# Kernel tuning notes

Hardware: AMD Instinct MI355X
Metric: run time of the kernel (lower is better)

Reference implementation:

```python
import jax, jax.numpy as jnp
import numpy as np

P_BINS = 5
T_BINS = 16
B_BINS = P_BINS * T_BINS  # 80
IN_CH = 16
OUT_CH = 32
N_VERTS = 30000   # mesh vertices (cols of conn)
N_PATCH = 30000   # patches (rows of conn / B)
K_NNZ = 3         # nnz per sparse row (interpolation support)


def setup_inputs() -> dict:
    key = jax.random.key(0)
    k1, k2, k3, k4 = jax.random.split(key, 4)
    x = jax.random.normal(k1, (N_VERTS, IN_CH), dtype=jnp.float32)
    conn_idx = jax.random.randint(k2, (N_PATCH * B_BINS, K_NNZ), 0, N_VERTS, dtype=jnp.int32)
    conn_val = jax.random.uniform(k3, (N_PATCH * B_BINS, K_NNZ), dtype=jnp.float32)
    weights = jax.random.normal(k4, (B_BINS, IN_CH, OUT_CH), dtype=jnp.float32)
    return {"x": x, "conn_idx": conn_idx, "conn_val": conn_val, "weights": weights}


def _rotated_weights(weights):
    # layer_weights[j, :, :, i] = weights[(j + p*i) % B]  -> reshape (B*inp, out*t)
    j = jnp.arange(B_BINS)[:, None]
    i = jnp.arange(T_BINS)[None, :]
    idx = (j + P_BINS * i) % B_BINS                       # (B, t)
    lw = weights[idx]                                     # (B, t, inp, out)
    lw = jnp.transpose(lw, (0, 2, 3, 1))                  # (B, inp, out, t)
    return lw.reshape(B_BINS * IN_CH, OUT_CH * T_BINS)


def reference(x, conn_idx, conn_val, weights):
    # sparse.mm(conn, x): gather K vertex features per bin row and weight-sum
    gathered = jnp.einsum('rk,rkc->rc', conn_val, x[conn_idx])  # (N*B, inp)
    h = gathered.reshape(-1, B_BINS * IN_CH)                    # (N, B*inp)
    lw = _rotated_weights(weights)                              # (B*inp, out*t)
    y = h @ lw                                                  # (N, out*t)
    y = y.reshape(-1, OUT_CH, T_BINS)
    return jnp.max(y, axis=-1)                                  # (N, out)
```

## Files before the change

kernel.cpp:

```cpp
#include <hip/hip_runtime.h>
#include <hip/hip_bf16.h>
#include <stdint.h>

#define NP 30000
#define BBINS 80
#define INCH 16
#define OUTCH 32
#define KDIM 1280
#define NDIM 512
#define KSTEPS 40
#define NROWS (NP * BBINS)

typedef __bf16 bf16x8 __attribute__((ext_vector_type(8)));
typedef __bf16 bf16x4 __attribute__((ext_vector_type(4)));
typedef float f32x4 __attribute__((ext_vector_type(4)));

__device__ __forceinline__ void async_ld16(const void* g, void* l) {
    __builtin_amdgcn_global_load_lds(
        (const __attribute__((address_space(1))) unsigned int*)g,
        (__attribute__((address_space(3))) unsigned int*)l,
        16, 0, 0);
}

__global__ void prep_weights(const float* __restrict__ w, __bf16* __restrict__ pw) {
    int gid = blockIdx.x * 256 + threadIdx.x;
    int e  = gid & 7;
    int qs = (gid >> 3) & 3;
    int n  = (gid >> 5) & 511;
    int kc = gid >> 14;
    int kp = kc * 32 + ((qs ^ (n & 3)) << 3) + e;
    int b = kp >> 4, c = kp & 15;
    int o = n >> 4,  t = n & 15;
    int bid = (b + 5 * t) % BBINS;
    pw[gid] = (__bf16)w[(bid * INCH + c) * OUTCH + o];
}

__global__ __launch_bounds__(256) void gather_h(
    const float* __restrict__ x,
    const int*   __restrict__ cidx,
    const float* __restrict__ cval,
    __bf16* __restrict__ h) {
    const int gid = blockIdx.x * 256 + threadIdx.x;
    const int r = gid >> 2;
    const int q = gid & 3;
    const int r3 = r * 3;
    const int i0 = cidx[r3 + 0], i1 = cidx[r3 + 1], i2 = cidx[r3 + 2];
    const float v0 = cval[r3 + 0], v1 = cval[r3 + 1], v2 = cval[r3 + 2];
    const float4 a = *(const float4*)(x + (size_t)i0 * 16 + q * 4);
    const float4 b = *(const float4*)(x + (size_t)i1 * 16 + q * 4);
    const float4 c = *(const float4*)(x + (size_t)i2 * 16 + q * 4);
    bf16x4 hv;
    hv[0] = (__bf16)(v0 * a.x + v1 * b.x + v2 * c.x);
    hv[1] = (__bf16)(v0 * a.y + v1 * b.y + v2 * c.y);
    hv[2] = (__bf16)(v0 * a.z + v1 * b.z + v2 * c.z);
    hv[3] = (__bf16)(v0 * a.w + v1 * b.w + v2 * c.w);
    *(bf16x4*)((char*)h + (size_t)gid * 8) = hv;
}

__global__ __launch_bounds__(256, 2) void gemm_max(
    const __bf16* __restrict__ h,
    const __bf16* __restrict__ pw,
    float* __restrict__ out) {

    __shared__ __align__(16) __bf16 Alds[128 * 32];
    __shared__ __align__(16) __bf16 Blds[256 * 32];

    const int bid = blockIdx.x;
    const int m    = (bid >> 4) * 8 + (bid & 7);
    const int ncol = (bid >> 3) & 1;
    if (m >= 235) return;
    const int mbase = m * 128;

    const int tid  = threadIdx.x;
    const int lane = tid & 63;
    const int wave = tid >> 6;
    const int wave_mrow = wave >> 1;
    const int wave_ncol = wave & 1;

    int a_off[4], b_off[8];
    {
        const int ml = lane & 15, q = lane >> 4;
#pragma unroll
        for (int i = 0; i < 4; ++i)
            a_off[i] = (wave_mrow * 64 + i * 16 + ml) * 64 + q * 16;
#pragma unroll
        for (int j = 0; j < 8; ++j) {
            int nl = wave_ncol * 128 + j * 16 + ml;
            b_off[j] = nl * 64 + ((q ^ (nl & 3)) << 4);
        }
    }

    f32x4 acc[4][8];
#pragma unroll
    for (int i = 0; i < 4; ++i)
#pragma unroll
        for (int j = 0; j < 8; ++j)
            acc[i][j] = (f32x4){0.f, 0.f, 0.f, 0.f};

    const char* hB  = (const char*)h;
    const char* pwB = (const char*)pw + ncol * 16384 + tid * 16;
    int rg0 = mbase + (tid >> 2);
    int rg1 = rg0 + 64;
    if (rg0 > NP - 1) rg0 = NP - 1;
    if (rg1 > NP - 1) rg1 = NP - 1;
    const char* aSrc0 = hB + (size_t)rg0 * 2560 + (tid & 3) * 16;
    const char* aSrc1 = hB + (size_t)rg1 * 2560 + (tid & 3) * 16;
    char* aDst0 = (char*)Alds + tid * 16;
    char* aDst1 = aDst0 + 4096;
    char* bDst  = (char*)Blds + tid * 16;

    for (int kc = 0; kc < KSTEPS; ++kc) {
        const char* bs = pwB + kc * 32768;
#pragma unroll
        for (int i = 0; i < 4; ++i)
            async_ld16(bs + i * 4096, bDst + i * 4096);
        async_ld16(aSrc0 + kc * 64, aDst0);
        async_ld16(aSrc1 + kc * 64, aDst1);
        __syncthreads();

        bf16x8 af[4], bfr[8];
#pragma unroll
        for (int i = 0; i < 4; ++i)
            af[i] = *(const bf16x8*)((const char*)Alds + a_off[i]);
#pragma unroll
        for (int j = 0; j < 8; ++j)
            bfr[j] = *(const bf16x8*)((const char*)Blds + b_off[j]);
#pragma unroll
        for (int i = 0; i < 4; ++i)
#pragma unroll
            for (int j = 0; j < 8; ++j)
                acc[i][j] = __builtin_amdgcn_mfma_f32_16x16x32_bf16(
                    af[i], bfr[j], acc[i][j], 0, 0, 0);
        __syncthreads();
    }

    const int rgrp = lane >> 4;
    const int tl   = lane & 15;
#pragma unroll
    for (int i = 0; i < 4; ++i) {
#pragma unroll
        for (int j = 0; j < 8; ++j) {
            float v0 = acc[i][j][0], v1 = acc[i][j][1];
            float v2 = acc[i][j][2], v3 = acc[i][j][3];
#pragma unroll
            for (int off = 1; off < 16; off <<= 1) {
                v0 = fmaxf(v0, __shfl_xor(v0, off));
                v1 = fmaxf(v1, __shfl_xor(v1, off));
                v2 = fmaxf(v2, __shfl_xor(v2, off));
                v3 = fmaxf(v3, __shfl_xor(v3, off));
            }
            if (tl == 0) {
                const int o  = ncol * 16 + wave_ncol * 8 + j;
                const int pr = mbase + wave_mrow * 64 + i * 16 + rgrp * 4;
                if (pr + 0 < NP) out[(pr + 0) * 32 + o] = v0;
                if (pr + 1 < NP) out[(pr + 1) * 32 + o] = v1;
                if (pr + 2 < NP) out[(pr + 2) * 32 + o] = v2;
                if (pr + 3 < NP) out[(pr + 3) * 32 + o] = v3;
            }
        }
    }
}

extern "C" void kernel_launch(void* const* d_in, const int* in_sizes, int n_in,
                              void* d_out, int out_size, void* d_ws, size_t ws_size,
                              hipStream_t stream) {
    const float* x    = (const float*)d_in[0];
    const int*   cidx = (const int*)d_in[1];
    const float* cval = (const float*)d_in[2];
    const float* w    = (const float*)d_in[3];
    float* out = (float*)d_out;

    __bf16* pw = (__bf16*)d_ws;
    __bf16* h  = (__bf16*)((char*)d_ws + (2 << 20));

    hipLaunchKernelGGL(prep_weights, dim3(2560), dim3(256), 0, stream, w, pw);
    hipLaunchKernelGGL(gather_h, dim3(NROWS * 4 / 256), dim3(256), 0, stream,
                       x, cidx, cval, h);
    hipLaunchKernelGGL(gemm_max, dim3(480), dim3(256), 0, stream,
                       h, (const __bf16*)pw, out);
}
```

Before: 188.8 us.

## Double-buffer GEMM LDS stages, enlarge tiles, swizzle A layout, stage gather indices in LDS

The GEMM now uses 512-thread blocks over 256-row tiles, with double-buffered A and B LDS stages, so each k-step's async loads overlap the previous step's MFMAs and one barrier per iteration is removed. The gather kernel loads each block's index and value rows into shared memory with coalesced vector loads. It also writes h in a swizzled order so A-fragment LDS reads avoid bank conflicts, and the weight swizzle is changed to the same pattern. The cost is a single barrier guarding buffer reuse, which leaves subtle races possible, plus more LDS per block, which may lower occupancy.

Result: slower. 209.9 us (+11.1%).

```diff
diff --git a/kernel.cpp b/kernel.cpp
--- a/kernel.cpp
+++ b/kernel.cpp
@@ -28,7 +28,7 @@
     int qs = (gid >> 3) & 3;
     int n  = (gid >> 5) & 511;
     int kc = gid >> 14;
-    int kp = kc * 32 + ((qs ^ (n & 3)) << 3) + e;
+    int kp = kc * 32 + ((qs ^ ((n >> 1) & 3)) << 3) + e;
     int b = kp >> 4, c = kp & 15;
     int o = n >> 4,  t = n & 15;
     int bid = (b + 5 * t) % BBINS;
@@ -40,12 +40,22 @@
     const int*   __restrict__ cidx,
     const float* __restrict__ cval,
     __bf16* __restrict__ h) {
-    const int gid = blockIdx.x * 256 + threadIdx.x;
-    const int r = gid >> 2;
-    const int q = gid & 3;
-    const int r3 = r * 3;
-    const int i0 = cidx[r3 + 0], i1 = cidx[r3 + 1], i2 = cidx[r3 + 2];
-    const float v0 = cval[r3 + 0], v1 = cval[r3 + 1], v2 = cval[r3 + 2];
+    __shared__ int   ci[192];
+    __shared__ float cv[192];
+    const int t  = threadIdx.x;
+    const int r0 = blockIdx.x * 64;
+
+    if (t < 48)
+        ((int4*)ci)[t] = ((const int4*)(cidx + (size_t)r0 * 3))[t];
+    else if (t >= 64 && t < 112)
+        ((float4*)cv)[t - 64] = ((const float4*)(cval + (size_t)r0 * 3))[t - 64];
+    __syncthreads();
+
+    const int rl = t >> 2;
+    const int q  = t & 3;
+    const int i0 = ci[rl * 3 + 0], i1 = ci[rl * 3 + 1], i2 = ci[rl * 3 + 2];
+    const float v0 = cv[rl * 3 + 0], v1 = cv[rl * 3 + 1], v2 = cv[rl * 3 + 2];
+
     const float4 a = *(const float4*)(x + (size_t)i0 * 16 + q * 4);
     const float4 b = *(const float4*)(x + (size_t)i1 * 16 + q * 4);
     const float4 c = *(const float4*)(x + (size_t)i2 * 16 + q * 4);
@@ -54,40 +64,44 @@
     hv[1] = (__bf16)(v0 * a.y + v1 * b.y + v2 * c.y);
     hv[2] = (__bf16)(v0 * a.z + v1 * b.z + v2 * c.z);
     hv[3] = (__bf16)(v0 * a.w + v1 * b.w + v2 * c.w);
-    *(bf16x4*)((char*)h + (size_t)gid * 8) = hv;
-}
-
-__global__ __launch_bounds__(256, 2) void gemm_max(
+
+    const int r   = r0 + rl;
+    const int p   = r / 80;
+    const int bin = r - p * 80;
+    const int cl  = 2 * (bin & 1) + (q >> 1);
+    const int slot = cl ^ ((p >> 1) & 3);
+    const size_t off = (size_t)p * 2560 + (bin >> 1) * 64 + slot * 16 + (q & 1) * 8;
+    *(bf16x4*)((char*)h + off) = hv;
+}
+
+__global__ __launch_bounds__(512, 2) void gemm_max(
     const __bf16* __restrict__ h,
     const __bf16* __restrict__ pw,
     float* __restrict__ out) {
 
-    __shared__ __align__(16) __bf16 Alds[128 * 32];
-    __shared__ __align__(16) __bf16 Blds[256 * 32];
-
-    const int bid = blockIdx.x;
-    const int m    = (bid >> 4) * 8 + (bid & 7);
-    const int ncol = (bid >> 3) & 1;
-    if (m >= 235) return;
-    const int mbase = m * 128;
+    __shared__ __align__(16) char Abuf[2][16384];
+    __shared__ __align__(16) char Bbuf[2][16384];
+
+    const int m    = blockIdx.x >> 1;
+    const int ncol = blockIdx.x & 1;
+    const int mbase = m * 256;
 
     const int tid  = threadIdx.x;
     const int lane = tid & 63;
     const int wave = tid >> 6;
-    const int wave_mrow = wave >> 1;
-    const int wave_ncol = wave & 1;
+    const int wm = wave >> 1;
+    const int wc = wave & 1;
 
     int a_off[4], b_off[8];
     {
         const int ml = lane & 15, q = lane >> 4;
+        const int swz = (q ^ ((ml >> 1) & 3)) << 4;
 #pragma unroll
         for (int i = 0; i < 4; ++i)
-            a_off[i] = (wave_mrow * 64 + i * 16 + ml) * 64 + q * 16;
-#pragma unroll
-        for (int j = 0; j < 8; ++j) {
-            int nl = wave_ncol * 128 + j * 16 + ml;
-            b_off[j] = nl * 64 + ((q ^ (nl & 3)) << 4);
-        }
+            a_off[i] = (wm * 64 + i * 16 + ml) * 64 + swz;
+#pragma unroll
+        for (int j = 0; j < 8; ++j)
+            b_off[j] = (wc * 128 + j * 16 + ml) * 64 + swz;
     }
 
     f32x4 acc[4][8];
@@ -97,42 +111,47 @@
         for (int j = 0; j < 8; ++j)
             acc[i][j] = (f32x4){0.f, 0.f, 0.f, 0.f};
 
-    const char* hB  = (const char*)h;
-    const char* pwB = (const char*)pw + ncol * 16384 + tid * 16;
-    int rg0 = mbase + (tid >> 2);
-    int rg1 = rg0 + 64;
-    if (rg0 > NP - 1) rg0 = NP - 1;
-    if (rg1 > NP - 1) rg1 = NP - 1;
-    const char* aSrc0 = hB + (size_t)rg0 * 2560 + (tid & 3) * 16;
-    const char* aSrc1 = hB + (size_t)rg1 * 2560 + (tid & 3) * 16;
-    char* aDst0 = (char*)Alds + tid * 16;
-    char* aDst1 = aDst0 + 4096;
-    char* bDst  = (char*)Blds + tid * 16;
+    int rA0 = mbase + (tid >> 2);
+    int rA1 = rA0 + 128;
+    if (rA0 > NP - 1) rA0 = NP - 1;
+    if (rA1 > NP - 1) rA1 = NP - 1;
+    const char* aSrc0 = (const char*)h + (size_t)rA0 * 2560 + (tid & 3) * 16;
+    const char* aSrc1 = (const char*)h + (size_t)rA1 * 2560 + (tid & 3) * 16;
+    const char* bSrc  = (const char*)pw + ncol * 16384 + tid * 16;
+    const int ldsOff  = tid * 16;
+
+#define STAGE(KC, BUF)                                                  \
+    do {                                                                \
+        async_ld16(aSrc0 + (KC) * 64, Abuf[BUF] + ldsOff);              \
+        async_ld16(aSrc1 + (KC) * 64, Abuf[BUF] + 8192 + ldsOff);       \
+        async_ld16(bSrc + (KC) * 32768, Bbuf[BUF] + ldsOff);            \
+        async_ld16(bSrc + (KC) * 32768 + 8192, Bbuf[BUF] + 8192 + ldsOff); \
+    } while (0)
+
+    STAGE(0, 0);
 
     for (int kc = 0; kc < KSTEPS; ++kc) {
-        const char* bs = pwB + kc * 32768;
+        __syncthreads();
+        if (kc + 1 < KSTEPS)
+            STAGE(kc + 1, (kc + 1) & 1);
+
+        const char* Ab = Abuf[kc & 1];
+        const char* Bb = Bbuf[kc & 1];
+        bf16x8 af[4], bfr[8];
 #pragma unroll
         for (int i = 0; i < 4; ++i)
-            async_ld16(bs + i * 4096, bDst + i * 4096);
-        async_ld16(aSrc0 + kc * 64, aDst0);
-        async_ld16(aSrc1 + kc * 64, aDst1);
-        __syncthreads();
-
-        bf16x8 af[4], bfr[8];
-#pragma unroll
-        for (int i = 0; i < 4; ++i)
-            af[i] = *(const bf16x8*)((const char*)Alds + a_off[i]);
+            af[i] = *(const bf16x8*)(Ab + a_off[i]);
 #pragma unroll
         for (int j = 0; j < 8; ++j)
-            bfr[j] = *(const bf16x8*)((const char*)Blds + b_off[j]);
+            bfr[j] = *(const bf16x8*)(Bb + b_off[j]);
 #pragma unroll
         for (int i = 0; i < 4; ++i)
 #pragma unroll
             for (int j = 0; j < 8; ++j)
                 acc[i][j] = __builtin_amdgcn_mfma_f32_16x16x32_bf16(
                     af[i], bfr[j], acc[i][j], 0, 0, 0);
-        __syncthreads();
     }
+#undef STAGE
 
     const int rgrp = lane >> 4;
     const int tl   = lane & 15;
@@ -150,8 +169,8 @@
                 v3 = fmaxf(v3, __shfl_xor(v3, off));
             }
             if (tl == 0) {
-                const int o  = ncol * 16 + wave_ncol * 8 + j;
-                const int pr = mbase + wave_mrow * 64 + i * 16 + rgrp * 4;
+                const int o  = ncol * 16 + wc * 8 + j;
+                const int pr = mbase + wm * 64 + i * 16 + rgrp * 4;
                 if (pr + 0 < NP) out[(pr + 0) * 32 + o] = v0;
                 if (pr + 1 < NP) out[(pr + 1) * 32 + o] = v1;
                 if (pr + 2 < NP) out[(pr + 2) * 32 + o] = v2;
@@ -174,8 +193,8 @@
     __bf16* h  = (__bf16*)((char*)d_ws + (2 << 20));
 
     hipLaunchKernelGGL(prep_weights, dim3(2560), dim3(256), 0, stream, w, pw);
-    hipLaunchKernelGGL(gather_h, dim3(NROWS * 4 / 256), dim3(256), 0, stream,
+    hipLaunchKernelGGL(gather_h, dim3(NROWS / 64), dim3(256), 0, stream,
                        x, cidx, cval, h);
-    hipLaunchKernelGGL(gemm_max, dim3(480), dim3(256), 0, stream,
+    hipLaunchKernelGGL(gemm_max, dim3(((NP + 255) / 256) * 2), dim3(512), 0, stream,
                        h, (const __bf16*)pw, out);
 }
```
